# Kernel tuning notes

Hardware: AMD Instinct MI355X
Metric: run time of the kernel (lower is better)

The kernel has to match this reference:

```python
import jax, jax.numpy as jnp
import numpy as np

T, D, N, K, H = 4096, 2560, 8, 4, 256
QUERY_PRE_ATTN_SCALAR = 256.0
ROPE_THETA = 10000.0
RMS_EPS = 1e-6
SLIDING_WINDOW = 1024
NEG_INF = -1e30


def setup_inputs() -> dict:
    key = jax.random.key(0)
    ks = jax.random.split(key, 6)
    return {
        "x": jax.random.normal(ks[0], (T, D), dtype=jnp.float32),
        "wq": jax.random.normal(ks[1], (D, N, H), dtype=jnp.float32) * 0.02,
        "wk": jax.random.normal(ks[2], (D, K, H), dtype=jnp.float32) * 0.02,
        "wv": jax.random.normal(ks[3], (D, K, H), dtype=jnp.float32) * 0.02,
        "wo": jax.random.normal(ks[4], (N, H, D), dtype=jnp.float32) * 0.02,
        "q_norm_w": jnp.ones((H,), dtype=jnp.float32),
        "k_norm_w": jnp.ones((H,), dtype=jnp.float32),
        "positions": jnp.arange(T, dtype=jnp.int32),
    }


def rms_norm(x, w, eps=RMS_EPS):
    rms = jnp.sqrt(jnp.mean(x * x, axis=-1, keepdims=True) + eps)
    return w * (x / rms)


def apply_rope(x, positions, head_dim, theta):
    # x: [T, heads, H]; rotate-half RoPE
    half = head_dim // 2
    inv_freq = theta ** (-(jnp.arange(half, dtype=jnp.float32) * 2.0 / head_dim))
    ang = positions.astype(jnp.float32)[:, None] * inv_freq  # [T, half]
    sin = jnp.sin(ang)[:, None, :]
    cos = jnp.cos(ang)[:, None, :]
    x1, x2 = jnp.split(x, 2, axis=-1)
    return jnp.concatenate([x1 * cos - x2 * sin, x2 * cos + x1 * sin], axis=-1)


def reference(x, wq, wk, wv, wo, q_norm_w, k_norm_w, positions):
    # QKV projections (per-head)
    q = jnp.einsum('td,dnh->tnh', x, wq)            # [T, N, H]
    q = rms_norm(q, q_norm_w)
    q = q * (QUERY_PRE_ATTN_SCALAR ** -0.5)
    q = apply_rope(q, positions, H, ROPE_THETA)

    k = jnp.einsum('td,dkh->tkh', x, wk)            # [T, K, H]
    k = rms_norm(k, k_norm_w)
    k = apply_rope(k, positions, H, ROPE_THETA)

    v = jnp.einsum('td,dkh->tkh', x, wv)            # [T, K, H]

    # GQA sliding-window causal attention
    G = N // K
    qh = q.reshape(T, K, G, H)
    scores = jnp.einsum('tkgh,skh->kgts', qh, k)    # [K, G, T, T]
    pq = positions[:, None]
    pk = positions[None, :]
    mask = (pk <= pq) & (pq - pk < SLIDING_WINDOW)  # [T, T]
    scores = jnp.where(mask, scores, NEG_INF)
    p = jax.nn.softmax(scores, axis=-1)
    attn = jnp.einsum('kgts,skh->tkgh', p, v).reshape(T, N, H)

    o = jnp.einsum('tnh,nhd->td', attn, wo)         # [T, D]
    new_kv_cache = jnp.stack([k, v])                # [2, T, K, H]
    return new_kv_cache, o
```

## Files before the change

kernel.cpp:

```cpp
#include <hip/hip_runtime.h>
#include <stdint.h>

#define T_TOK 4096
#define DM    2560
#define NQ    8
#define NKV   4
#define HD    256
#define WIN   1024

using bf16x8 = __attribute__((ext_vector_type(8))) short;
using f32x4  = __attribute__((ext_vector_type(4))) float;
typedef unsigned short u16;

__device__ __forceinline__ u16 f2bf(float x) {
  union { float f; uint32_t u; } v; v.f = x;
  uint32_t u = v.u;
  return (u16)((u + 0x7fffu + ((u >> 16) & 1u)) >> 16);
}
__device__ __forceinline__ float bf2f(u16 b) {
  union { uint32_t u; float f; } v; v.u = ((uint32_t)b) << 16;
  return v.f;
}

__device__ __forceinline__ void async_cp16(const void* g, void* lds) {
  __builtin_amdgcn_global_load_lds(
      (const __attribute__((address_space(1))) uint32_t*)(uintptr_t)g,
      (__attribute__((address_space(3))) uint32_t*)(uint32_t)(uintptr_t)lds,
      16, 0, 0);
}

__global__ __launch_bounds__(256) void convert_f32_bf16(
    const float* __restrict__ in, u16* __restrict__ out, int n)
{
  for (int i = (blockIdx.x * 256 + threadIdx.x) * 4; i < n; i += gridDim.x * 256 * 4) {
    float4 v = *(const float4*)(in + i);
    ushort4 o;
    o.x = f2bf(v.x); o.y = f2bf(v.y); o.z = f2bf(v.z); o.w = f2bf(v.w);
    *(ushort4*)(out + i) = o;
  }
}

__global__ __launch_bounds__(256) void transpose_f32_bf16(
    const float* __restrict__ in, u16* __restrict__ out, int R, int C)
{
  __shared__ u16 tile[64][65];
  const int r0 = blockIdx.y * 64, c0 = blockIdx.x * 64;
  const int tr = threadIdx.x >> 6, tc = threadIdx.x & 63;
  #pragma unroll
  for (int i = 0; i < 16; ++i) {
    int r = tr + i * 4;
    tile[r][tc] = f2bf(in[(size_t)(r0 + r) * C + c0 + tc]);
  }
  __syncthreads();
  #pragma unroll
  for (int i = 0; i < 16; ++i) {
    int c = tr + i * 4;
    out[(size_t)(c0 + c) * R + r0 + tc] = tile[tc][c];
  }
}

template<bool F32OUT>
__global__ __launch_bounds__(512, 1) void gemm256p(
    const u16* __restrict__ A, const u16* __restrict__ B, void* __restrict__ Cv,
    int Kd, int lda, int ldb, int ldc)
{
  __shared__ __align__(16) u16 lds[2][2][256 * 64];
  const int tid = threadIdx.x;
  const int wave = tid >> 6, lane = tid & 63;
  const int lg = lane >> 4, lc = lane & 15;
  const int wr = wave >> 2, wc = wave & 3;
  const int nwg = gridDim.x, bid = blockIdx.x;
  const int nid = (bid & 7) * (nwg >> 3) + (bid >> 3);
  const int m0 = (nid & 15) * 256, n0 = (nid >> 4) * 256;
  const int NT = Kd >> 6;

  const int srow = tid >> 3;
  const int scol = ((tid & 7) * 16) ^ ((srow & 7) << 4);
  const u16* Ag = A + (size_t)(m0 + srow) * lda + (scol >> 1);
  const u16* Bg = B + (size_t)(n0 + srow) * ldb + (scol >> 1);

  #define STAGE_B4(BUF, KT) do {                                              \
    const int kc_ = (KT) * 64;                                                \
    _Pragma("unroll")                                                         \
    for (int li = 0; li < 4; ++li)                                            \
      async_cp16(Bg + (size_t)(li * 64) * ldb + kc_,                          \
                 (char*)&lds[BUF][1][0] + li * 8192 + wave * 1024);           \
  } while (0)
  #define STAGE_A2(BUF, KT, H) do {                                           \
    const int kc_ = (KT) * 64;                                                \
    async_cp16(Ag + (size_t)((H) * 64) * lda + kc_,                           \
               (char*)&lds[BUF][0][0] + (H) * 8192 + wave * 1024);            \
    async_cp16(Ag + (size_t)((H) * 64 + 128) * lda + kc_,                     \
               (char*)&lds[BUF][0][0] + ((H) + 2) * 8192 + wave * 1024);      \
  } while (0)

  #define LOAD_AF(P) do {                                                     \
    _Pragma("unroll")                                                         \
    for (int im = 0; im < 2; ++im)                                            \
      _Pragma("unroll")                                                       \
      for (int k2 = 0; k2 < 2; ++k2) {                                        \
        const int row = wr * 128 + ((P) * 2 + im) * 16 + lc;                  \
        const int cb = k2 * 64 + lg * 16;                                     \
        af[im][k2] = *(const bf16x8*)(Ab + row * 128 + (cb ^ ((row & 7) << 4))); \
      }                                                                       \
  } while (0)
  #define MFMA_Q(P) do {                                                      \
    __builtin_amdgcn_s_setprio(1);                                            \
    _Pragma("unroll")                                                         \
    for (int im = 0; im < 2; ++im)                                            \
      _Pragma("unroll")                                                       \
      for (int j = 0; j < 4; ++j)                                             \
        _Pragma("unroll")                                                     \
        for (int k2 = 0; k2 < 2; ++k2)                                        \
          acc[(P) * 2 + im][j] = __builtin_amdgcn_mfma_f32_16x16x32_bf16(     \
              af[im][k2], bfr[j][k2], acc[(P) * 2 + im][j], 0, 0, 0);         \
    __builtin_amdgcn_s_setprio(0);                                            \
  } while (0)
  #define LGKM0_BAR() do {                                                    \
    asm volatile("s_waitcnt lgkmcnt(0)" ::: "memory");                        \
    __builtin_amdgcn_s_barrier();                                             \
    __builtin_amdgcn_sched_barrier(0);                                        \
  } while (0)

  const f32x4 zf = {0.f, 0.f, 0.f, 0.f};
  f32x4 acc[8][4];
  #pragma unroll
  for (int i = 0; i < 8; ++i)
    #pragma unroll
    for (int j = 0; j < 4; ++j) acc[i][j] = zf;

  STAGE_B4(0, 0); STAGE_A2(0, 0, 0); STAGE_A2(0, 0, 1);
  STAGE_B4(1, 1); STAGE_A2(1, 1, 0); STAGE_A2(1, 1, 1);
  asm volatile("s_waitcnt vmcnt(8)" ::: "memory");
  __builtin_amdgcn_s_barrier();
  __builtin_amdgcn_sched_barrier(0);

  for (int t = 0; t < NT; ++t) {
    const int cur = t & 1;
    const char* Ab = (const char*)&lds[cur][0][0];
    const char* Bb = (const char*)&lds[cur][1][0];
    int nk = t + 2; if (nk > NT - 1) nk = NT - 1;

    bf16x8 bfr[4][2], af[2][2];
    #pragma unroll
    for (int j = 0; j < 4; ++j)
      #pragma unroll
      for (int k2 = 0; k2 < 2; ++k2) {
        const int row = wc * 64 + j * 16 + lc;
        const int cb = k2 * 64 + lg * 16;
        bfr[j][k2] = *(const bf16x8*)(Bb + row * 128 + (cb ^ ((row & 7) << 4)));
      }
    LOAD_AF(0);
    LGKM0_BAR();
    STAGE_B4(cur, nk);
    MFMA_Q(0);
    LOAD_AF(1);
    LGKM0_BAR();
    STAGE_A2(cur, nk, 0);
    MFMA_Q(1);
    LOAD_AF(2);
    MFMA_Q(2);
    LOAD_AF(3);
    LGKM0_BAR();
    STAGE_A2(cur, nk, 1);
    MFMA_Q(3);
    asm volatile("s_waitcnt vmcnt(8)" ::: "memory");
    __builtin_amdgcn_s_barrier();
    __builtin_amdgcn_sched_barrier(0);
  }
  #undef STAGE_B4
  #undef STAGE_A2
  #undef LOAD_AF
  #undef MFMA_Q
  #undef LGKM0_BAR

  #pragma unroll
  for (int i = 0; i < 8; ++i)
    #pragma unroll
    for (int j = 0; j < 4; ++j)
      #pragma unroll
      for (int r = 0; r < 4; ++r) {
        const int row = m0 + wr * 128 + i * 16 + lg * 4 + r;
        const int col = n0 + wc * 64 + j * 16 + lc;
        if (F32OUT) ((float*)Cv)[(size_t)row * ldc + col] = acc[i][j][r];
        else        ((u16*)Cv)[(size_t)row * ldc + col] = f2bf(acc[i][j][r]);
      }
}

template<int BM, int BN, bool F32OUT>
__global__ __launch_bounds__(512, 2) void gemm_t(
    const u16* __restrict__ A, const u16* __restrict__ B, void* __restrict__ Cv,
    int Kd, int lda, int ldb, int ldc, int MT)
{
  constexpr int MF = BM / 32;
  constexpr int NF = BN / 64;
  constexpr int ISS = (BM + BN) / 64;
  constexpr int AISS = BM / 64;
  __shared__ __align__(16) u16 lds[2][(BM + BN) * 64];
  const int tid = threadIdx.x;
  const int wave = tid >> 6, lane = tid & 63;
  const int lg = lane >> 4, lc = lane & 15;
  const int wr = wave >> 2, wc = wave & 3;
  const int nwg = gridDim.x, bid = blockIdx.x;
  const int nid = (bid & 7) * (nwg >> 3) + (bid >> 3);
  const int m0 = (nid % MT) * BM, n0 = (nid / MT) * BN;
  const int NT = Kd >> 6;

  const int srow = tid >> 3;
  const int scol = ((tid & 7) * 16) ^ ((srow & 7) << 4);
  const u16* Ag = A + (size_t)(m0 + srow) * lda + (scol >> 1);
  const u16* Bg = B + (size_t)(n0 + srow) * ldb + (scol >> 1);
  char* lds0 = (char*)&lds[0][0];
  char* lds1 = (char*)&lds[1][0];

  #define STAGE_T(LD, KT) do {                                              \
    const int kc_ = (KT) * 64;                                              \
    _Pragma("unroll")                                                       \
    for (int li = 0; li < ISS; ++li) {                                      \
      if (li < AISS)                                                        \
        async_cp16(Ag + (size_t)(li * 64) * lda + kc_,                      \
                   (LD) + li * 8192 + wave * 1024);                         \
      else                                                                  \
        async_cp16(Bg + (size_t)((li - AISS) * 64) * ldb + kc_,             \
                   (LD) + li * 8192 + wave * 1024);                         \
    }                                                                       \
  } while (0)

  #define WAIT_ISS() do {                                                   \
    if (ISS == 8) asm volatile("s_waitcnt vmcnt(8)" ::: "memory");          \
    else          asm volatile("s_waitcnt vmcnt(7)" ::: "memory");          \
  } while (0)

  const f32x4 zf = {0.f, 0.f, 0.f, 0.f};
  f32x4 acc[MF][NF];
  #pragma unroll
  for (int i = 0; i < MF; ++i)
    #pragma unroll
    for (int j = 0; j < NF; ++j) acc[i][j] = zf;

  STAGE_T(lds0, 0);
  STAGE_T(lds1, 1);
  WAIT_ISS();
  __builtin_amdgcn_s_barrier();
  __builtin_amdgcn_sched_barrier(0);

  for (int t = 0; t < NT; ++t) {
    const int cur = t & 1;
    const char* Ab = cur ? lds1 : lds0;
    const char* Bb = Ab + BM * 128;

    bf16x8 bf[NF][2];
    #pragma unroll
    for (int j = 0; j < NF; ++j)
      #pragma unroll
      for (int k2 = 0; k2 < 2; ++k2) {
        const int row = wc * (BN / 4) + j * 16 + lc;
        const int cb = k2 * 64 + lg * 16;
        bf[j][k2] = *(const bf16x8*)(Bb + row * 128 + (cb ^ ((row & 7) << 4)));
      }

    #pragma unroll
    for (int p = 0; p < MF / 2; ++p) {
      bf16x8 af[2][2];
      #pragma unroll
      for (int im = 0; im < 2; ++im)
        #pragma unroll
        for (int k2 = 0; k2 < 2; ++k2) {
          const int row = wr * (BM / 2) + (p * 2 + im) * 16 + lc;
          const int cb = k2 * 64 + lg * 16;
          af[im][k2] = *(const bf16x8*)(Ab + row * 128 + (cb ^ ((row & 7) << 4)));
        }
      __builtin_amdgcn_s_setprio(1);
      #pragma unroll
      for (int im = 0; im < 2; ++im)
        #pragma unroll
        for (int j = 0; j < NF; ++j)
          #pragma unroll
          for (int k2 = 0; k2 < 2; ++k2)
            acc[p * 2 + im][j] = __builtin_amdgcn_mfma_f32_16x16x32_bf16(
                af[im][k2], bf[j][k2], acc[p * 2 + im][j], 0, 0, 0);
      __builtin_amdgcn_s_setprio(0);
    }

    __builtin_amdgcn_s_barrier();
    __builtin_amdgcn_sched_barrier(0);
    int nk = t + 2; if (nk > NT - 1) nk = NT - 1;
    if (cur == 0) { STAGE_T(lds0, nk); } else { STAGE_T(lds1, nk); }
    WAIT_ISS();
    __builtin_amdgcn_s_barrier();
    __builtin_amdgcn_sched_barrier(0);
  }
  #undef STAGE_T
  #undef WAIT_ISS

  #pragma unroll
  for (int i = 0; i < MF; ++i)
    #pragma unroll
    for (int j = 0; j < NF; ++j)
      #pragma unroll
      for (int r = 0; r < 4; ++r) {
        const int row = m0 + wr * (BM / 2) + i * 16 + lg * 4 + r;
        const int col = n0 + wc * (BN / 4) + j * 16 + lc;
        if (F32OUT) ((float*)Cv)[(size_t)row * ldc + col] = acc[i][j][r];
        else        ((u16*)Cv)[(size_t)row * ldc + col] = f2bf(acc[i][j][r]);
      }
}

__global__ __launch_bounds__(256) void fuse_norm_rope(
    const u16* __restrict__ qkv, const float* __restrict__ qnw, const float* __restrict__ knw,
    const int* __restrict__ pos, u16* __restrict__ qb, u16* __restrict__ kb,
    u16* __restrict__ vb, float* __restrict__ kvout)
{
  const int t = blockIdx.x;
  const int wave = threadIdx.x >> 6, lane = threadIdx.x & 63;
  const float p = (float)pos[t];
  const float kf = 0.10381025296523007f;
  float s0, c0, s1, c1;
  sincosf(p * exp2f(-(float)lane * kf), &s0, &c0);
  sincosf(p * exp2f(-(float)(lane + 64) * kf), &s1, &c1);
  const u16* row = qkv + (size_t)t * 4096;

  for (int pp = 0; pp < 4; ++pp) {
    const int hr = pp * 4 + wave;
    if (hr >= 12) {
      const int kk = hr - 12;
      const u16* src = row + 3072 + kk * 256;
      float* dstf = kvout + (size_t)T_TOK * NKV * HD + ((size_t)t * NKV + kk) * HD;
      u16*   dstb = vb + ((size_t)t * NKV + kk) * HD;
      #pragma unroll
      for (int q4 = 0; q4 < 4; ++q4) {
        const u16 s = src[lane + q4 * 64];
        dstf[lane + q4 * 64] = bf2f(s);
        dstb[lane + q4 * 64] = s;
      }
    } else {
      const bool isq = hr < 8;
      const int cb = isq ? hr * 256 : 2048 + (hr - 8) * 256;
      float v0 = bf2f(row[cb + lane]);
      float v1 = bf2f(row[cb + lane + 64]);
      float v2 = bf2f(row[cb + lane + 128]);
      float v3 = bf2f(row[cb + lane + 192]);
      float ss = v0 * v0 + v1 * v1 + v2 * v2 + v3 * v3;
      #pragma unroll
      for (int off = 1; off < 64; off <<= 1) ss += __shfl_xor(ss, off);
      float sc = rsqrtf(ss * (1.0f / 256.0f) + 1e-6f);
      if (isq) sc *= 0.0625f;
      const float* wn = isq ? qnw : knw;
      v0 *= sc * wn[lane];
      v1 *= sc * wn[lane + 64];
      v2 *= sc * wn[lane + 128];
      v3 *= sc * wn[lane + 192];
      const float n0 = v0 * c0 - v2 * s0;
      const float n2 = v2 * c0 + v0 * s0;
      const float n1 = v1 * c1 - v3 * s1;
      const float n3 = v3 * c1 + v1 * s1;
      if (isq) {
        u16* dst = qb + (size_t)t * 2048 + hr * 256;
        dst[lane]       = f2bf(n0);
        dst[lane + 64]  = f2bf(n1);
        dst[lane + 128] = f2bf(n2);
        dst[lane + 192] = f2bf(n3);
      } else {
        const int kk = hr - 8;
        float* dstf = kvout + ((size_t)t * NKV + kk) * HD;
        dstf[lane]       = n0;
        dstf[lane + 64]  = n1;
        dstf[lane + 128] = n2;
        dstf[lane + 192] = n3;
        u16* dstb = kb + ((size_t)t * NKV + kk) * HD;
        dstb[lane]       = f2bf(n0);
        dstb[lane + 64]  = f2bf(n1);
        dstb[lane + 128] = f2bf(n2);
        dstb[lane + 192] = f2bf(n3);
      }
    }
  }
}

__global__ __launch_bounds__(256) void transpose_v(
    const u16* __restrict__ vc, u16* __restrict__ vt)
{
  __shared__ u16 tile[64][65];
  const int kk = blockIdx.z;
  const int t0 = blockIdx.y * 64, h0 = blockIdx.x * 64;
  const int tr = threadIdx.x >> 6, tc = threadIdx.x & 63;
  #pragma unroll
  for (int i = 0; i < 16; ++i) {
    int tt = tr + i * 4;
    tile[tt][tc] = vc[((size_t)(t0 + tt) * NKV + kk) * HD + h0 + tc];
  }
  __syncthreads();
  #pragma unroll
  for (int i = 0; i < 16; ++i) {
    int h = tr + i * 4;
    vt[(size_t)kk * HD * T_TOK + (size_t)(h0 + h) * T_TOK + t0 + tc] = tile[tc][h];
  }
}

__global__ __launch_bounds__(512, 1) void attn_kernel(
    const u16* __restrict__ qb, const u16* __restrict__ kc,
    const u16* __restrict__ vt, u16* __restrict__ ob)
{
  __shared__ __align__(16) u16 Ks[2][64 * 256];
  __shared__ __align__(16) u16 Vts[2][256 * 64];
  __shared__ __align__(16) u16 Ps[8][16 * 64];

  const int kk = blockIdx.y;
  const int t0 = blockIdx.x * 64;
  const int tid = threadIdx.x;
  const int wave = tid >> 6, lane = tid & 63;
  const int lg = lane >> 4, lc = lane & 15;
  const int hq = kk * 2 + (wave >> 2);
  const int wrow = (wave & 3) * 16;
  const int lswz = (lc & 7) << 4;
  const f32x4 zf = {0.f, 0.f, 0.f, 0.f};

  const int lrowK = tid >> 5;
  const int scolK = ((tid & 31) * 16) ^ ((lrowK & 7) << 4);
  const int lrowV = tid >> 3;
  const int scolV = ((tid & 7) * 16) ^ ((lrowV & 7) << 4);

  #define STAGEKV(KT, BUF) do {                                                \
    const int kb_ = (KT) * 64;                                                 \
    const u16* kp_ = kc + (size_t)(kb_ + lrowK) * (NKV * HD) + kk * HD + (scolK >> 1); \
    _Pragma("unroll")                                                          \
    for (int is = 0; is < 4; ++is)                                             \
      async_cp16(kp_ + (size_t)(is * 16) * (NKV * HD),                         \
                 (char*)&Ks[BUF][0] + is * 8192 + wave * 1024);                \
    const u16* vp_ = vt + (size_t)kk * (HD * T_TOK) + (size_t)lrowV * T_TOK + kb_ + (scolV >> 1); \
    _Pragma("unroll")                                                          \
    for (int is = 0; is < 4; ++is)                                             \
      async_cp16(vp_ + (size_t)(is * 64) * T_TOK,                              \
                 (char*)&Vts[BUF][0] + is * 8192 + wave * 1024);               \
  } while (0)

  bf16x8 qf[8];
  {
    const u16* qp = qb + (size_t)(t0 + wrow + lc) * 2048 + hq * 256 + lg * 8;
    #pragma unroll
    for (int ks = 0; ks < 8; ++ks) qf[ks] = *(const bf16x8*)(qp + ks * 32);
  }

  f32x4 o_acc[16];
  #pragma unroll
  for (int j = 0; j < 16; ++j) o_acc[j] = zf;
  float m_r[4], l_r[4];
  #pragma unroll
  for (int r = 0; r < 4; ++r) { m_r[r] = -1e30f; l_r[r] = 0.f; }

  const int mtile = t0 >> 6;
  const int ktf = (mtile >= 16) ? (mtile - 16) : 0;

  STAGEKV(ktf, 0);
  __syncthreads();

  int cur = 0;
  for (int kt = ktf; kt <= mtile; ++kt) {
    const int kb = kt * 64;
    if (kt < mtile) STAGEKV(kt + 1, cur ^ 1);

    const u16* Kb = &Ks[cur][0];
    const u16* Vb = &Vts[cur][0];

    f32x4 sf[4];
    #pragma unroll
    for (int j = 0; j < 4; ++j) sf[j] = zf;
    __builtin_amdgcn_s_setprio(1);
    #pragma unroll
    for (int ks = 0; ks < 8; ++ks)
      #pragma unroll
      for (int j = 0; j < 4; ++j) {
        const int row = j * 16 + lc;
        bf16x8 kf = *(const bf16x8*)((const char*)Kb + ((row * 512 + ks * 64 + lg * 16) ^ lswz));
        sf[j] = __builtin_amdgcn_mfma_f32_16x16x32_bf16(qf[ks], kf, sf[j], 0, 0, 0);
      }
    __builtin_amdgcn_s_setprio(0);

    const bool interior = (kb >= t0 - 960) && (kb <= t0 - 64);
    if (!interior) {
      #pragma unroll
      for (int j = 0; j < 4; ++j) {
        const int gcol = kb + j * 16 + lc;
        #pragma unroll
        for (int r = 0; r < 4; ++r) {
          const int grow = t0 + wrow + lg * 4 + r;
          if ((unsigned)(grow - gcol) >= WIN) sf[j][r] = -1e30f;
        }
      }
    }

    float a_r[4];
    #pragma unroll
    for (int r = 0; r < 4; ++r) {
      float v = fmaxf(fmaxf(sf[0][r], sf[1][r]), fmaxf(sf[2][r], sf[3][r]));
      v = fmaxf(v, __shfl_xor(v, 1));
      v = fmaxf(v, __shfl_xor(v, 2));
      v = fmaxf(v, __shfl_xor(v, 4));
      v = fmaxf(v, __shfl_xor(v, 8));
      const float mn = fmaxf(m_r[r], v);
      a_r[r] = __expf(m_r[r] - mn);
      m_r[r] = mn;
    }

    char* myP = (char*)&Ps[wave][0];
    #pragma unroll
    for (int r = 0; r < 4; ++r) {
      const int row = lg * 4 + r;
      const int rsw = (row & 7) << 4;
      float su = 0.f;
      #pragma unroll
      for (int j = 0; j < 4; ++j) {
        const float p = __expf(sf[j][r] - m_r[r]);
        su += p;
        *(u16*)(myP + ((row * 128 + (j * 16 + lc) * 2) ^ rsw)) = f2bf(p);
      }
      su += __shfl_xor(su, 1);
      su += __shfl_xor(su, 2);
      su += __shfl_xor(su, 4);
      su += __shfl_xor(su, 8);
      l_r[r] = l_r[r] * a_r[r] + su;
    }

    #pragma unroll
    for (int j = 0; j < 16; ++j) {
      o_acc[j][0] *= a_r[0];
      o_acc[j][1] *= a_r[1];
      o_acc[j][2] *= a_r[2];
      o_acc[j][3] *= a_r[3];
    }

    bf16x8 pa[2];
    #pragma unroll
    for (int ks = 0; ks < 2; ++ks)
      pa[ks] = *(const bf16x8*)(myP + ((lc * 128 + ks * 64 + lg * 16) ^ lswz));
    __builtin_amdgcn_s_setprio(1);
    #pragma unroll
    for (int ks = 0; ks < 2; ++ks)
      #pragma unroll
      for (int j = 0; j < 16; ++j) {
        const int row = j * 16 + lc;
        bf16x8 vf = *(const bf16x8*)((const char*)Vb + ((row * 128 + ks * 64 + lg * 16) ^ lswz));
        o_acc[j] = __builtin_amdgcn_mfma_f32_16x16x32_bf16(pa[ks], vf, o_acc[j], 0, 0, 0);
      }
    __builtin_amdgcn_s_setprio(0);

    __syncthreads();
    cur ^= 1;
  }
  #undef STAGEKV

  #pragma unroll
  for (int r = 0; r < 4; ++r) {
    const float li = 1.f / l_r[r];
    const size_t rowb = (size_t)(t0 + wrow + lg * 4 + r) * 2048 + hq * 256 + lc;
    #pragma unroll
    for (int j = 0; j < 16; ++j)
      ob[rowb + j * 16] = f2bf(o_acc[j][r] * li);
  }
}

extern "C" void kernel_launch(void* const* d_in, const int* in_sizes, int n_in,
                              void* d_out, int out_size, void* d_ws, size_t ws_size,
                              hipStream_t stream)
{
  (void)in_sizes; (void)n_in; (void)out_size; (void)ws_size;
  const float* x   = (const float*)d_in[0];
  const float* wq  = (const float*)d_in[1];
  const float* wk  = (const float*)d_in[2];
  const float* wv  = (const float*)d_in[3];
  const float* wo  = (const float*)d_in[4];
  const float* qnw = (const float*)d_in[5];
  const float* knw = (const float*)d_in[6];
  const int*   pos = (const int*)d_in[7];
  float* out = (float*)d_out;

  char* ws = (char*)d_ws;
  u16* woT   = (u16*)(ws);
  u16* xb    = (u16*)(ws + 10485760);
  u16* wqkvT = (u16*)(ws + 31457280);
  u16* qkv   = (u16*)(ws + 52428800);
  u16* q_b   = xb;
  u16* kb    = wqkvT;
  u16* vb    = (u16*)(ws + 31457280 + 8388608);
  u16* vtb   = qkv;
  u16* attn  = (u16*)(ws + 52428800 + 8388608);

  convert_f32_bf16<<<2048, 256, 0, stream>>>(x, xb, T_TOK * DM);
  transpose_f32_bf16<<<dim3(32, 40), 256, 0, stream>>>(wq, wqkvT, DM, 2048);
  transpose_f32_bf16<<<dim3(16, 40), 256, 0, stream>>>(wk, wqkvT + 2048 * DM, DM, 1024);
  transpose_f32_bf16<<<dim3(16, 40), 256, 0, stream>>>(wv, wqkvT + 3072 * DM, DM, 1024);
  transpose_f32_bf16<<<dim3(40, 32), 256, 0, stream>>>(wo, woT, 2048, DM);

  gemm256p<false><<<256, 512, 0, stream>>>(xb, wqkvT, qkv, DM, DM, DM, 4096);

  fuse_norm_rope<<<T_TOK, 256, 0, stream>>>(qkv, qnw, knw, pos, q_b, kb, vb, out);

  transpose_v<<<dim3(4, 64, 4), 256, 0, stream>>>(vb, vtb);

  attn_kernel<<<dim3(64, 4), 512, 0, stream>>>(q_b, kb, vtb, attn);

  gemm_t<128, 320, true><<<256, 512, 0, stream>>>(attn, woT, out + 2 * (size_t)T_TOK * NKV * HD,
                                                  2048, 2048, 2048, DM, 32);
}
```

Baseline: 251.5 us.

## Pipeline output-projection GEMM and vectorize conversion and transpose kernels

Replaces the templated output-projection GEMM with a specialized 128x320 kernel. The new kernel issues the next tile's global-to-LDS loads in halves, interleaved with the MFMA phases, instead of after a full barrier, and drops to one workgroup per CU. The f32-to-bf16 convert, the weight transposes and the V transpose now use 16-byte vector loads and stores with a padded LDS tile. The aim is to overlap memory traffic with compute in the GEMM and to cut memory transactions in the prep kernels. Reading LDS columns with a stride-72 pad may cause bank conflicts, and the lower occupancy risks exposing latency.

New measurement: 250.3 us. No clear change (-0.5%).

```diff
diff --git a/kernel.cpp b/kernel.cpp
--- a/kernel.cpp
+++ b/kernel.cpp
@@ -32,18 +32,22 @@
 __global__ __launch_bounds__(256) void convert_f32_bf16(
     const float* __restrict__ in, u16* __restrict__ out, int n)
 {
-  for (int i = (blockIdx.x * 256 + threadIdx.x) * 4; i < n; i += gridDim.x * 256 * 4) {
-    float4 v = *(const float4*)(in + i);
-    ushort4 o;
-    o.x = f2bf(v.x); o.y = f2bf(v.y); o.z = f2bf(v.z); o.w = f2bf(v.w);
-    *(ushort4*)(out + i) = o;
+  for (int i = (blockIdx.x * 256 + threadIdx.x) * 8; i < n; i += gridDim.x * 256 * 8) {
+    float4 a = *(const float4*)(in + i);
+    float4 b = *(const float4*)(in + i + 4);
+    bf16x8 o;
+    o[0] = (short)f2bf(a.x); o[1] = (short)f2bf(a.y);
+    o[2] = (short)f2bf(a.z); o[3] = (short)f2bf(a.w);
+    o[4] = (short)f2bf(b.x); o[5] = (short)f2bf(b.y);
+    o[6] = (short)f2bf(b.z); o[7] = (short)f2bf(b.w);
+    *(bf16x8*)(out + i) = o;
   }
 }
 
 __global__ __launch_bounds__(256) void transpose_f32_bf16(
     const float* __restrict__ in, u16* __restrict__ out, int R, int C)
 {
-  __shared__ u16 tile[64][65];
+  __shared__ u16 tile[64][72];
   const int r0 = blockIdx.y * 64, c0 = blockIdx.x * 64;
   const int tr = threadIdx.x >> 6, tc = threadIdx.x & 63;
   #pragma unroll
@@ -52,10 +56,14 @@
     tile[r][tc] = f2bf(in[(size_t)(r0 + r) * C + c0 + tc]);
   }
   __syncthreads();
-  #pragma unroll
-  for (int i = 0; i < 16; ++i) {
-    int c = tr + i * 4;
-    out[(size_t)(c0 + c) * R + r0 + tc] = tile[tc][c];
+  const int oc = threadIdx.x >> 3, ch = threadIdx.x & 7;
+  #pragma unroll
+  for (int h = 0; h < 2; ++h) {
+    const int c = oc + h * 32;
+    bf16x8 v;
+    #pragma unroll
+    for (int j = 0; j < 8; ++j) v[j] = (short)tile[ch * 8 + j][c];
+    *(bf16x8*)(out + (size_t)(c0 + c) * R + r0 + ch * 8) = v;
   }
 }
 
@@ -93,7 +101,6 @@
     async_cp16(Ag + (size_t)((H) * 64 + 128) * lda + kc_,                     \
                (char*)&lds[BUF][0][0] + ((H) + 2) * 8192 + wave * 1024);      \
   } while (0)
-
   #define LOAD_AF(P) do {                                                     \
     _Pragma("unroll")                                                         \
     for (int im = 0; im < 2; ++im)                                            \
@@ -187,122 +194,122 @@
       }
 }
 
-template<int BM, int BN, bool F32OUT>
-__global__ __launch_bounds__(512, 2) void gemm_t(
-    const u16* __restrict__ A, const u16* __restrict__ B, void* __restrict__ Cv,
-    int Kd, int lda, int ldb, int ldc, int MT)
-{
-  constexpr int MF = BM / 32;
-  constexpr int NF = BN / 64;
-  constexpr int ISS = (BM + BN) / 64;
-  constexpr int AISS = BM / 64;
-  __shared__ __align__(16) u16 lds[2][(BM + BN) * 64];
+__global__ __launch_bounds__(512, 1) void gemm_p2(
+    const u16* __restrict__ A, const u16* __restrict__ B, float* __restrict__ C,
+    int Kd, int lda, int ldb, int ldc)
+{
+  __shared__ __align__(16) u16 lds[2][(128 + 320) * 64];
   const int tid = threadIdx.x;
   const int wave = tid >> 6, lane = tid & 63;
   const int lg = lane >> 4, lc = lane & 15;
   const int wr = wave >> 2, wc = wave & 3;
   const int nwg = gridDim.x, bid = blockIdx.x;
   const int nid = (bid & 7) * (nwg >> 3) + (bid >> 3);
-  const int m0 = (nid % MT) * BM, n0 = (nid / MT) * BN;
+  const int m0 = (nid & 31) * 128, n0 = (nid >> 5) * 320;
   const int NT = Kd >> 6;
 
   const int srow = tid >> 3;
   const int scol = ((tid & 7) * 16) ^ ((srow & 7) << 4);
   const u16* Ag = A + (size_t)(m0 + srow) * lda + (scol >> 1);
   const u16* Bg = B + (size_t)(n0 + srow) * ldb + (scol >> 1);
-  char* lds0 = (char*)&lds[0][0];
-  char* lds1 = (char*)&lds[1][0];
-
-  #define STAGE_T(LD, KT) do {                                              \
-    const int kc_ = (KT) * 64;                                              \
-    _Pragma("unroll")                                                       \
-    for (int li = 0; li < ISS; ++li) {                                      \
-      if (li < AISS)                                                        \
-        async_cp16(Ag + (size_t)(li * 64) * lda + kc_,                      \
-                   (LD) + li * 8192 + wave * 1024);                         \
-      else                                                                  \
-        async_cp16(Bg + (size_t)((li - AISS) * 64) * ldb + kc_,             \
-                   (LD) + li * 8192 + wave * 1024);                         \
-    }                                                                       \
-  } while (0)
-
-  #define WAIT_ISS() do {                                                   \
-    if (ISS == 8) asm volatile("s_waitcnt vmcnt(8)" ::: "memory");          \
-    else          asm volatile("s_waitcnt vmcnt(7)" ::: "memory");          \
+
+  #define STAGE_B5(BUF, KT) do {                                              \
+    const int kc_ = (KT) * 64;                                                \
+    _Pragma("unroll")                                                         \
+    for (int li = 0; li < 5; ++li)                                            \
+      async_cp16(Bg + (size_t)(li * 64) * ldb + kc_,                          \
+                 (char*)&lds[BUF][0] + 16384 + li * 8192 + wave * 1024);      \
+  } while (0)
+  #define STAGE_A2P(BUF, KT) do {                                             \
+    const int kc_ = (KT) * 64;                                                \
+    _Pragma("unroll")                                                         \
+    for (int li = 0; li < 2; ++li)                                            \
+      async_cp16(Ag + (size_t)(li * 64) * lda + kc_,                          \
+                 (char*)&lds[BUF][0] + li * 8192 + wave * 1024);              \
+  } while (0)
+  #define LOAD_AF2(P) do {                                                    \
+    _Pragma("unroll")                                                         \
+    for (int im = 0; im < 2; ++im)                                            \
+      _Pragma("unroll")                                                       \
+      for (int k2 = 0; k2 < 2; ++k2) {                                        \
+        const int row = wr * 64 + ((P) * 2 + im) * 16 + lc;                   \
+        const int cb = k2 * 64 + lg * 16;                                     \
+        af[im][k2] = *(const bf16x8*)(Ab + row * 128 + (cb ^ ((row & 7) << 4))); \
+      }                                                                       \
+  } while (0)
+  #define MFMA_Q2(P) do {                                                     \
+    __builtin_amdgcn_s_setprio(1);                                            \
+    _Pragma("unroll")                                                         \
+    for (int im = 0; im < 2; ++im)                                            \
+      _Pragma("unroll")                                                       \
+      for (int j = 0; j < 5; ++j)                                             \
+        _Pragma("unroll")                                                     \
+        for (int k2 = 0; k2 < 2; ++k2)                                        \
+          acc[(P) * 2 + im][j] = __builtin_amdgcn_mfma_f32_16x16x32_bf16(     \
+              af[im][k2], bfr[j][k2], acc[(P) * 2 + im][j], 0, 0, 0);         \
+    __builtin_amdgcn_s_setprio(0);                                            \
+  } while (0)
+  #define LGKM0_BAR2() do {                                                   \
+    asm volatile("s_waitcnt lgkmcnt(0)" ::: "memory");                        \
+    __builtin_amdgcn_s_barrier();                                             \
+    __builtin_amdgcn_sched_barrier(0);                                        \
   } while (0)
 
   const f32x4 zf = {0.f, 0.f, 0.f, 0.f};
-  f32x4 acc[MF][NF];
-  #pragma unroll
-  for (int i = 0; i < MF; ++i)
-    #pragma unroll
-    for (int j = 0; j < NF; ++j) acc[i][j] = zf;
-
-  STAGE_T(lds0, 0);
-  STAGE_T(lds1, 1);
-  WAIT_ISS();
+  f32x4 acc[4][5];
+  #pragma unroll
+  for (int i = 0; i < 4; ++i)
+    #pragma unroll
+    for (int j = 0; j < 5; ++j) acc[i][j] = zf;
+
+  STAGE_B5(0, 0); STAGE_A2P(0, 0);
+  STAGE_B5(1, 1); STAGE_A2P(1, 1);
+  asm volatile("s_waitcnt vmcnt(7)" ::: "memory");
   __builtin_amdgcn_s_barrier();
   __builtin_amdgcn_sched_barrier(0);
 
   for (int t = 0; t < NT; ++t) {
     const int cur = t & 1;
-    const char* Ab = cur ? lds1 : lds0;
-    const char* Bb = Ab + BM * 128;
-
-    bf16x8 bf[NF][2];
-    #pragma unroll
-    for (int j = 0; j < NF; ++j)
+    const char* Ab = (const char*)&lds[cur][0];
+    const char* Bb = Ab + 16384;
+    int nk = t + 2; if (nk > NT - 1) nk = NT - 1;
+
+    bf16x8 bfr[5][2], af[2][2];
+    #pragma unroll
+    for (int j = 0; j < 5; ++j)
       #pragma unroll
       for (int k2 = 0; k2 < 2; ++k2) {
-        const int row = wc * (BN / 4) + j * 16 + lc;
+        const int row = wc * 80 + j * 16 + lc;
         const int cb = k2 * 64 + lg * 16;
-        bf[j][k2] = *(const bf16x8*)(Bb + row * 128 + (cb ^ ((row & 7) << 4)));
-      }
-
-    #pragma unroll
-    for (int p = 0; p < MF / 2; ++p) {
-      bf16x8 af[2][2];
-      #pragma unroll
-      for (int im = 0; im < 2; ++im)
-        #pragma unroll
-        for (int k2 = 0; k2 < 2; ++k2) {
-          const int row = wr * (BM / 2) + (p * 2 + im) * 16 + lc;
-          const int cb = k2 * 64 + lg * 16;
-          af[im][k2] = *(const bf16x8*)(Ab + row * 128 + (cb ^ ((row & 7) << 4)));
-        }
-      __builtin_amdgcn_s_setprio(1);
-      #pragma unroll
-      for (int im = 0; im < 2; ++im)
-        #pragma unroll
-        for (int j = 0; j < NF; ++j)
-          #pragma unroll
-          for (int k2 = 0; k2 < 2; ++k2)
-            acc[p * 2 + im][j] = __builtin_amdgcn_mfma_f32_16x16x32_bf16(
-                af[im][k2], bf[j][k2], acc[p * 2 + im][j], 0, 0, 0);
-      __builtin_amdgcn_s_setprio(0);
-    }
-
+        bfr[j][k2] = *(const bf16x8*)(Bb + row * 128 + (cb ^ ((row & 7) << 4)));
+      }
+    LOAD_AF2(0);
+    LGKM0_BAR2();
+    STAGE_B5(cur, nk);
+    MFMA_Q2(0);
+    LOAD_AF2(1);
+    LGKM0_BAR2();
+    STAGE_A2P(cur, nk);
+    MFMA_Q2(1);
+    asm volatile("s_waitcnt vmcnt(7)" ::: "memory");
     __builtin_amdgcn_s_barrier();
     __builtin_amdgcn_sched_barrier(0);
-    int nk = t + 2; if (nk > NT - 1) nk = NT - 1;
-    if (cur == 0) { STAGE_T(lds0, nk); } else { STAGE_T(lds1, nk); }
-    WAIT_ISS();
-    __builtin_amdgcn_s_barrier();
-    __builtin_amdgcn_sched_barrier(0);
-  }
-  #undef STAGE_T
-  #undef WAIT_ISS
-
-  #pragma unroll
-  for (int i = 0; i < MF; ++i)
-    #pragma unroll
-    for (int j = 0; j < NF; ++j)
+  }
+  #undef STAGE_B5
+  #undef STAGE_A2P
+  #undef LOAD_AF2
+  #undef MFMA_Q2
+  #undef LGKM0_BAR2
+
+  #pragma unroll
+  for (int i = 0; i < 4; ++i)
+    #pragma unroll
+    for (int j = 0; j < 5; ++j)
       #pragma unroll
       for (int r = 0; r < 4; ++r) {
-        const int row = m0 + wr * (BM / 2) + i * 16 + lg * 4 + r;
-        const int col = n0 + wc * (BN / 4) + j * 16 + lc;
-        if (F32OUT) ((float*)Cv)[(size_t)row * ldc + col] = acc[i][j][r];
-        else        ((u16*)Cv)[(size_t)row * ldc + col] = f2bf(acc[i][j][r]);
+        const int row = m0 + wr * 64 + i * 16 + lg * 4 + r;
+        const int col = n0 + wc * 80 + j * 16 + lc;
+        C[(size_t)row * ldc + col] = acc[i][j][r];
       }
 }
 
@@ -380,20 +387,24 @@
 __global__ __launch_bounds__(256) void transpose_v(
     const u16* __restrict__ vc, u16* __restrict__ vt)
 {
-  __shared__ u16 tile[64][65];
+  __shared__ u16 tile[64][72];
   const int kk = blockIdx.z;
   const int t0 = blockIdx.y * 64, h0 = blockIdx.x * 64;
-  const int tr = threadIdx.x >> 6, tc = threadIdx.x & 63;
-  #pragma unroll
-  for (int i = 0; i < 16; ++i) {
-    int tt = tr + i * 4;
-    tile[tt][tc] = vc[((size_t)(t0 + tt) * NKV + kk) * HD + h0 + tc];
+  const int lr = threadIdx.x >> 3, ch = threadIdx.x & 7;
+  #pragma unroll
+  for (int h = 0; h < 2; ++h) {
+    const int row = lr + h * 32;
+    *(bf16x8*)&tile[row][ch * 8] =
+        *(const bf16x8*)&vc[((size_t)(t0 + row) * NKV + kk) * HD + h0 + ch * 8];
   }
   __syncthreads();
   #pragma unroll
-  for (int i = 0; i < 16; ++i) {
-    int h = tr + i * 4;
-    vt[(size_t)kk * HD * T_TOK + (size_t)(h0 + h) * T_TOK + t0 + tc] = tile[tc][h];
+  for (int h = 0; h < 2; ++h) {
+    const int hc = lr + h * 32;
+    bf16x8 v;
+    #pragma unroll
+    for (int j = 0; j < 8; ++j) v[j] = (short)tile[ch * 8 + j][hc];
+    *(bf16x8*)&vt[(size_t)kk * HD * T_TOK + (size_t)(h0 + hc) * T_TOK + t0 + ch * 8] = v;
   }
 }
 
@@ -585,7 +596,7 @@
   u16* vtb   = qkv;
   u16* attn  = (u16*)(ws + 52428800 + 8388608);
 
-  convert_f32_bf16<<<2048, 256, 0, stream>>>(x, xb, T_TOK * DM);
+  convert_f32_bf16<<<1024, 256, 0, stream>>>(x, xb, T_TOK * DM);
   transpose_f32_bf16<<<dim3(32, 40), 256, 0, stream>>>(wq, wqkvT, DM, 2048);
   transpose_f32_bf16<<<dim3(16, 40), 256, 0, stream>>>(wk, wqkvT + 2048 * DM, DM, 1024);
   transpose_f32_bf16<<<dim3(16, 40), 256, 0, stream>>>(wv, wqkvT + 3072 * DM, DM, 1024);
@@ -599,6 +610,6 @@
 
   attn_kernel<<<dim3(64, 4), 512, 0, stream>>>(q_b, kb, vtb, attn);
 
-  gemm_t<128, 320, true><<<256, 512, 0, stream>>>(attn, woT, out + 2 * (size_t)T_TOK * NKV * HD,
-                                                  2048, 2048, 2048, DM, 32);
-}
+  gemm_p2<<<256, 512, 0, stream>>>(attn, woT, out + 2 * (size_t)T_TOK * NKV * HD,
+                                   2048, 2048, 2048, DM);
+}
```
